# Kernel tuning notes

Measured on AMD Instinct MI355X. Metric: run time of the kernel, lower is better.

The kernel has to match this reference:

```python
import jax, jax.numpy as jnp
import numpy as np

N = 4_000_000      # total rows across all strata
D = 64             # covariate dimension (nn.Linear input_size)
N_SEG = 100_000    # number of strata (groups)


def setup_inputs() -> dict:
    key = jax.random.key(0)
    k1, k2, k3, k4 = jax.random.split(key, 4)
    X = jax.random.normal(k1, (N, D), dtype=jnp.float32)
    # sorted segment ids encode the ragged strata lengths (rows are packed per group)
    seg_ids = jnp.sort(jax.random.randint(k2, (N,), 0, N_SEG)).astype(jnp.int32)
    w = jax.random.normal(k3, (D,), dtype=jnp.float32) * 0.1
    b = jax.random.normal(k4, (1,), dtype=jnp.float32)
    return {"X": X, "seg_ids": seg_ids, "w": w, "b": b}


def reference(X, seg_ids, w, b):
    # linear projection to a single logit per row: y_hat = X @ w + b
    logits = X @ w + b[0]                                   # [N]
    # segment softmax == padded (-300) row softmax with padding underflowing to 0
    m = jax.ops.segment_max(logits, seg_ids, num_segments=N_SEG)   # [N_SEG]
    m = jnp.where(jnp.isfinite(m), m, jnp.float32(0.0))            # guard empty segments
    z = jnp.exp(logits - m[seg_ids])                               # [N]
    denom = jax.ops.segment_sum(z, seg_ids, num_segments=N_SEG)    # [N_SEG]
    return z / denom[seg_ids]                                      # [N] per-group softmax probs
```

## Files before the change

kernel.cpp:

```cpp
#include <hip/hip_runtime.h>
#include <math.h>

#define NROWS 4000000
#define DCOV  64
#define NSEG  100000

#define SEGS_PER_BLOCK 25
#define NBLOCKS (NSEG / SEGS_PER_BLOCK)
#define CAP 2048

typedef float f32x4 __attribute__((ext_vector_type(4)));

__global__ __launch_bounds__(256, 8)
void fused_clr_kernel(const float* __restrict__ X,
                      const int* __restrict__ seg,
                      const float* __restrict__ w,
                      const float* __restrict__ b,
                      float* __restrict__ out,
                      float* __restrict__ gl ) {
    __shared__ int   st_lds[SEGS_PER_BLOCK + 1];
    __shared__ float logit_lds[CAP];
    __shared__ int   rs_sh, re_sh;

    const int tid  = threadIdx.x;
    const int lane = tid & 63;
    const int wv   = tid >> 6;
    const int sub  = lane & 15;
    const int rig  = lane >> 4;

    const int s0 = blockIdx.x * SEGS_PER_BLOCK;
    const int s1 = s0 + SEGS_PER_BLOCK;

    if (tid < 2) {
        const int target = (tid == 0) ? s0 : s1;
        int lo = 0, hi = NROWS;
        while (lo < hi) {
            int mid = (lo + hi) >> 1;
            if (seg[mid] < target) lo = mid + 1; else hi = mid;
        }
        if (tid == 0) rs_sh = lo; else re_sh = lo;
    }
    __syncthreads();
    const int row_start = rs_sh;
    const int row_end   = re_sh;
    const int nrows     = row_end - row_start;

    for (int j = tid; j <= SEGS_PER_BLOCK; j += 256) st_lds[j] = row_end;
    __syncthreads();
    for (int i = row_start + tid; i < row_end; i += 256) {
        int s    = seg[i];
        int prev = (i == row_start) ? (s0 - 1) : seg[i - 1];
        for (int t = prev + 1; t <= s; ++t) st_lds[t - s0] = i;
    }

    const bool  use_lds = (nrows <= CAP);
    const float bias    = b[0];
    const float4 w4     = reinterpret_cast<const float4*>(w)[sub];
    const f32x4* Xv     = reinterpret_cast<const f32x4*>(X);

    __syncthreads();

    for (int rb = row_start + wv * 16; rb < row_end; rb += 64) {
        const int r0 = rb + rig, r1 = rb + 4 + rig, r2 = rb + 8 + rig, r3 = rb + 12 + rig;
        f32x4 x0 = {0,0,0,0}, x1 = {0,0,0,0}, x2 = {0,0,0,0}, x3 = {0,0,0,0};
        const f32x4* xp = Xv + (long long)rb * 16 + lane;
        if (r0 < row_end) x0 = __builtin_nontemporal_load(xp);
        if (r1 < row_end) x1 = __builtin_nontemporal_load(xp + 64);
        if (r2 < row_end) x2 = __builtin_nontemporal_load(xp + 128);
        if (r3 < row_end) x3 = __builtin_nontemporal_load(xp + 192);
        float p0 = x0.x * w4.x + x0.y * w4.y + x0.z * w4.z + x0.w * w4.w;
        float p1 = x1.x * w4.x + x1.y * w4.y + x1.z * w4.z + x1.w * w4.w;
        float p2 = x2.x * w4.x + x2.y * w4.y + x2.z * w4.z + x2.w * w4.w;
        float p3 = x3.x * w4.x + x3.y * w4.y + x3.z * w4.z + x3.w * w4.w;
        #pragma unroll
        for (int m = 1; m < 16; m <<= 1) {
            p0 += __shfl_xor(p0, m);
            p1 += __shfl_xor(p1, m);
            p2 += __shfl_xor(p2, m);
            p3 += __shfl_xor(p3, m);
        }
        if (sub == 0) {
            if (use_lds) {
                if (r0 < row_end) logit_lds[r0 - row_start] = p0 + bias;
                if (r1 < row_end) logit_lds[r1 - row_start] = p1 + bias;
                if (r2 < row_end) logit_lds[r2 - row_start] = p2 + bias;
                if (r3 < row_end) logit_lds[r3 - row_start] = p3 + bias;
            } else {
                if (r0 < row_end) gl[r0] = p0 + bias;
                if (r1 < row_end) gl[r1] = p1 + bias;
                if (r2 < row_end) gl[r2] = p2 + bias;
                if (r3 < row_end) gl[r3] = p3 + bias;
            }
        }
    }
    __syncthreads();

    for (int j = wv; j < SEGS_PER_BLOCK; j += 4) {
        const int a0  = st_lds[j];
        const int a1  = st_lds[j + 1];
        const int len = a1 - a0;
        if (len <= 0) continue;
        if (len <= 64) {
            const bool act = lane < len;
            const int  idx = a0 - row_start + lane;
            float x = act ? (use_lds ? logit_lds[idx] : gl[a0 + lane]) : -INFINITY;
            float mx = x;
            #pragma unroll
            for (int m = 1; m < 64; m <<= 1) mx = fmaxf(mx, __shfl_xor(mx, m));
            float e = act ? __expf(x - mx) : 0.0f;
            float sum = e;
            #pragma unroll
            for (int m = 1; m < 64; m <<= 1) sum += __shfl_xor(sum, m);
            const float pr = e / sum;
            if (act) {
                if (use_lds) logit_lds[idx] = pr;
                else         out[a0 + lane] = pr;
            }
        } else {
            float mx = -INFINITY;
            for (int i = a0 + lane; i < a1; i += 64)
                mx = fmaxf(mx, use_lds ? logit_lds[i - row_start] : gl[i]);
            #pragma unroll
            for (int m = 1; m < 64; m <<= 1) mx = fmaxf(mx, __shfl_xor(mx, m));
            float sum = 0.0f;
            for (int i = a0 + lane; i < a1; i += 64)
                sum += __expf((use_lds ? logit_lds[i - row_start] : gl[i]) - mx);
            #pragma unroll
            for (int m = 1; m < 64; m <<= 1) sum += __shfl_xor(sum, m);
            const float inv = 1.0f / sum;
            for (int i = a0 + lane; i < a1; i += 64) {
                float pr = __expf((use_lds ? logit_lds[i - row_start] : gl[i]) - mx) * inv;
                if (use_lds) logit_lds[i - row_start] = pr;
                else         out[i] = pr;
            }
        }
    }
    __syncthreads();

    if (use_lds) {
        for (int i = tid; i < nrows; i += 256)
            out[row_start + i] = logit_lds[i];
    }
}

extern "C" void kernel_launch(void* const* d_in, const int* in_sizes, int n_in,
                              void* d_out, int out_size, void* d_ws, size_t ws_size,
                              hipStream_t stream) {
    const float* X   = (const float*)d_in[0];
    const int*   seg = (const int*)d_in[1];
    const float* w   = (const float*)d_in[2];
    const float* b   = (const float*)d_in[3];
    float*       out = (float*)d_out;
    float*       gl  = (float*)d_ws;

    fused_clr_kernel<<<NBLOCKS, 256, 0, stream>>>(X, seg, w, b, out, gl);
}
```

Before: 185.4 us.

## Use wave-parallel segment search, drop barriers and LDS write-back pass

Replaces the single-thread binary search for block row bounds with a wave-cooperative 64-ary search that uses ballot/popcount, cutting the serial dependent-load latency at block start. The segment-start table initialization is merged into the boundary scan, which removes a barrier. Softmax results are now written straight to global memory with nontemporal stores, which removes the final barrier and the LDS copy-out loop. Each segment's probabilities are still written by a single wave, so the extra stores are cheap, but the search now issues 64 loads per step instead of one.

```diff
diff --git a/kernel.cpp b/kernel.cpp
--- a/kernel.cpp
+++ b/kernel.cpp
@@ -10,6 +10,21 @@
 #define CAP 2048
 
 typedef float f32x4 __attribute__((ext_vector_type(4)));
+
+__device__ __forceinline__ int lower_bound_seg(const int* __restrict__ seg,
+                                               int target, int lane) {
+    int lo = 0, n = NROWS;
+    while (n > 64) {
+        const int step = (n + 63) >> 6;
+        const long long p = (long long)lo + (long long)(lane + 1) * step;
+        const bool lt = (p < (long long)lo + n) && (seg[p] < target);
+        const int cnt = (int)__popcll(__ballot(lt));
+        lo += cnt * step;
+        n = min(step, n - cnt * step);
+    }
+    const bool lt = (lane < n) && (seg[lo + lane] < target);
+    return lo + (int)__popcll(__ballot(lt));
+}
 
 __global__ __launch_bounds__(256, 8)
 void fused_clr_kernel(const float* __restrict__ X,
@@ -31,34 +46,35 @@
     const int s0 = blockIdx.x * SEGS_PER_BLOCK;
     const int s1 = s0 + SEGS_PER_BLOCK;
 
-    if (tid < 2) {
-        const int target = (tid == 0) ? s0 : s1;
-        int lo = 0, hi = NROWS;
-        while (lo < hi) {
-            int mid = (lo + hi) >> 1;
-            if (seg[mid] < target) lo = mid + 1; else hi = mid;
-        }
-        if (tid == 0) rs_sh = lo; else re_sh = lo;
+    if (wv == 0) {
+        int r = lower_bound_seg(seg, s0, lane);
+        if (lane == 0) rs_sh = r;
+    } else if (wv == 1) {
+        int r = lower_bound_seg(seg, s1, lane);
+        if (lane == 0) re_sh = r;
     }
     __syncthreads();
     const int row_start = rs_sh;
     const int row_end   = re_sh;
     const int nrows     = row_end - row_start;
 
-    for (int j = tid; j <= SEGS_PER_BLOCK; j += 256) st_lds[j] = row_end;
-    __syncthreads();
-    for (int i = row_start + tid; i < row_end; i += 256) {
-        int s    = seg[i];
-        int prev = (i == row_start) ? (s0 - 1) : seg[i - 1];
-        for (int t = prev + 1; t <= s; ++t) st_lds[t - s0] = i;
-    }
-
     const bool  use_lds = (nrows <= CAP);
     const float bias    = b[0];
     const float4 w4     = reinterpret_cast<const float4*>(w)[sub];
     const f32x4* Xv     = reinterpret_cast<const f32x4*>(X);
 
-    __syncthreads();
+    if (nrows == 0) {
+        if (tid <= SEGS_PER_BLOCK) st_lds[tid] = row_end;
+    } else {
+        for (int i = row_start + tid; i < row_end; i += 256) {
+            const int s    = seg[i];
+            const int prev = (i == row_start) ? (s0 - 1) : seg[i - 1];
+            for (int t = prev + 1; t <= s; ++t) st_lds[t - s0] = i;
+            if (i == row_end - 1) {
+                for (int t = s + 1; t <= s1; ++t) st_lds[t - s0] = row_end;
+            }
+        }
+    }
 
     for (int rb = row_start + wv * 16; rb < row_end; rb += 64) {
         const int r0 = rb + rig, r1 = rb + 4 + rig, r2 = rb + 8 + rig, r3 = rb + 12 + rig;
@@ -111,11 +127,7 @@
             float sum = e;
             #pragma unroll
             for (int m = 1; m < 64; m <<= 1) sum += __shfl_xor(sum, m);
-            const float pr = e / sum;
-            if (act) {
-                if (use_lds) logit_lds[idx] = pr;
-                else         out[a0 + lane] = pr;
-            }
+            if (act) __builtin_nontemporal_store(e / sum, &out[a0 + lane]);
         } else {
             float mx = -INFINITY;
             for (int i = a0 + lane; i < a1; i += 64)
@@ -130,16 +142,9 @@
             const float inv = 1.0f / sum;
             for (int i = a0 + lane; i < a1; i += 64) {
                 float pr = __expf((use_lds ? logit_lds[i - row_start] : gl[i]) - mx) * inv;
-                if (use_lds) logit_lds[i - row_start] = pr;
-                else         out[i] = pr;
+                __builtin_nontemporal_store(pr, &out[i]);
             }
         }
-    }
-    __syncthreads();
-
-    if (use_lds) {
-        for (int i = tid; i < nrows; i += 256)
-            out[row_start + i] = logit_lds[i];
     }
 }
 
```

Result: no change. 183.3 us (-1.1%).
